# Performance work log

Hardware: AMD Instinct MI355X
Metric: run time of the kernel (lower is better)

Reference implementation:

```python
import jax, jax.numpy as jnp
import numpy as np

V, D, H, L, S, W = 32000, 1024, 16, 2, 2048, 256
HD = D // H
SCALE = 1.0 / np.sqrt(HD)
NEG = -1e30
EPS = 1e-5


def setup_inputs() -> dict:
    key = jax.random.key(0)
    ks = jax.random.split(key, 16)
    f = lambda k, shape, s=0.02: (jax.random.normal(k, shape, jnp.float32) * s)
    return {
        'input_ids': jax.random.randint(ks[0], (1, S), 0, V, jnp.int32),
        'emb': f(ks[1], (V, D)),                 # token embedding, tied lm_head
        'pos_emb': f(ks[2], (S, D)),
        'wq': f(ks[3], (L, D, D)), 'bq': jnp.zeros((L, D), jnp.float32),
        'wk': f(ks[4], (L, D, D)), 'bk': jnp.zeros((L, D), jnp.float32),
        'wv': f(ks[5], (L, D, D)), 'bv': jnp.zeros((L, D), jnp.float32),
        'wo': f(ks[6], (L, D, D)), 'bo': jnp.zeros((L, D), jnp.float32),
        'w1': f(ks[7], (L, D, 4 * D)), 'b1': jnp.zeros((L, 4 * D), jnp.float32),
        'w2': f(ks[8], (L, 4 * D, D)), 'b2': jnp.zeros((L, D), jnp.float32),
        'ln1_g': jnp.ones((L, D), jnp.float32), 'ln1_b': jnp.zeros((L, D), jnp.float32),
        'ln2_g': jnp.ones((L, D), jnp.float32), 'ln2_b': jnp.zeros((L, D), jnp.float32),
        'out_g': jnp.ones((D,), jnp.float32), 'out_b': jnp.zeros((D,), jnp.float32),
    }


def _ln(x, g, b):
    mu = jnp.mean(x, axis=-1, keepdims=True)
    var = jnp.mean(jnp.square(x - mu), axis=-1, keepdims=True)
    return (x - mu) * jax.lax.rsqrt(var + EPS) * g + b


def _forward(input_ids, emb, pos_emb, wq, bq, wk, bk, wv, bv, wo, bo,
             w1, b1, w2, b2, ln1_g, ln1_b, ln2_g, ln2_b, out_g, out_b):
    B, seq = input_ids.shape
    x = emb[input_ids] + pos_emb[None, :seq]  # [B,S,D]
    idx = jnp.arange(seq)
    local_mask = jnp.abs(idx[:, None] - idx[None, :]) <= (W // 2)  # [S,S] band
    for l in range(L):
        h = _ln(x, ln1_g[l], ln1_b[l])
        q = (h @ wq[l] + bq[l]).reshape(B, seq, H, HD)
        k = (h @ wk[l] + bk[l]).reshape(B, seq, H, HD)
        v = (h @ wv[l] + bv[l]).reshape(B, seq, H, HD)
        scores = jnp.einsum('bqhd,bkhd->bhqk', q, k) * SCALE
        scores = jnp.where(local_mask[None, None], scores, NEG)
        attn = jax.nn.softmax(scores, axis=-1)
        o = jnp.einsum('bhqk,bkhd->bqhd', attn, v).reshape(B, seq, D)
        x = x + (o @ wo[l] + bo[l])
        h2 = _ln(x, ln2_g[l], ln2_b[l])
        ffn = jax.nn.gelu(h2 @ w1[l] + b1[l], approximate=False) @ w2[l] + b2[l]
        x = x + ffn
    x = _ln(x, out_g, out_b)
    logits = x @ emb.T  # tied lm_head, no bias
    return logits


def reference(input_ids, emb, pos_emb, wq, bq, wk, bk, wv, bv, wo, bo,
              w1, b1, w2, b2, ln1_g, ln1_b, ln2_g, ln2_b, out_g, out_b):
    return _forward(input_ids, emb, pos_emb, wq, bq, wk, bk, wv, bv, wo, bo,
                    w1, b1, w2, b2, ln1_g, ln1_b, ln2_g, ln2_b, out_g, out_b)
```

## Files before the change

kernel.cpp:

```cpp
#include <hip/hip_runtime.h>
#include <hip/hip_bf16.h>
#include <math.h>

#define SEQ    2048
#define DMODEL 1024
#define NHEAD  16
#define HDIM   64
#define NLAYER 2
#define VOCAB  32000
#define HALFW  128

typedef float  f32x4  __attribute__((ext_vector_type(4)));
typedef short  s16x8  __attribute__((ext_vector_type(8)));

__device__ __forceinline__ unsigned bf16_rne(float x) {
    unsigned b = __builtin_bit_cast(unsigned, x);
    return (b + 0x7FFFu + ((b >> 16) & 1u)) >> 16;
}
__device__ __forceinline__ unsigned pack2(float lo, float hi) {
    return bf16_rne(lo) | (bf16_rne(hi) << 16);
}
__device__ __forceinline__ void gl_lds16(const void* g, void* l) {
    __builtin_amdgcn_global_load_lds(
        (const __attribute__((address_space(1))) unsigned*)g,
        (__attribute__((address_space(3))) unsigned*)l, 16, 0, 0);
}

__global__ __launch_bounds__(256) void embed_kernel(
    const int* __restrict__ ids, const float* __restrict__ emb,
    const float* __restrict__ pos, float* __restrict__ X)
{
    const int s = blockIdx.x;
    const int t = threadIdx.x;
    const int id = ids[s];
    f32x4 e = *(const f32x4*)(emb + (size_t)id * DMODEL + t * 4);
    f32x4 p = *(const f32x4*)(pos + (size_t)s  * DMODEL + t * 4);
    *(f32x4*)(X + (size_t)s * DMODEL + t * 4) = e + p;
}

__global__ __launch_bounds__(256) void convert_bf16_kernel(
    const float* __restrict__ X, unsigned short* __restrict__ Y)
{
    const size_t i = (size_t)blockIdx.x * 256 + threadIdx.x;
    f32x4 a = *(const f32x4*)(X + i * 8);
    f32x4 b = *(const f32x4*)(X + i * 8 + 4);
    uint4 u = make_uint4(pack2(a.x, a.y), pack2(a.z, a.w),
                         pack2(b.x, b.y), pack2(b.z, b.w));
    *(uint4*)(Y + i * 8) = u;
}

__global__ __launch_bounds__(256) void transpose_bf16_kernel(
    const float* __restrict__ W, unsigned short* __restrict__ Wt, int K, int N)
{
    __shared__ unsigned short tile[64][65];
    const int k0 = blockIdx.x * 64;
    const int n0 = blockIdx.y * 64;
    const int t = threadIdx.x;
    const int tr = t >> 6;
    const int tc = t & 63;
    #pragma unroll
    for (int i = 0; i < 16; ++i) {
        int r = i * 4 + tr;
        tile[r][tc] = (unsigned short)bf16_rne(W[(size_t)(k0 + r) * N + n0 + tc]);
    }
    __syncthreads();
    #pragma unroll
    for (int i = 0; i < 16; ++i) {
        int r = i * 4 + tr;
        Wt[(size_t)(n0 + r) * K + k0 + tc] = tile[tc][r];
    }
}

__global__ __launch_bounds__(256) void pack3_kernel(
    const float* __restrict__ a, const float* __restrict__ b,
    const float* __restrict__ c, float* __restrict__ out)
{
    const int i = blockIdx.x * 256 + threadIdx.x;
    float v = (i < 1024) ? a[i] : (i < 2048 ? b[i - 1024] : c[i - 2048]);
    out[i] = v;
}

__global__ __launch_bounds__(256) void ln_bf16_kernel(
    const float* __restrict__ X, const float* __restrict__ G,
    const float* __restrict__ Bb, unsigned short* __restrict__ Y)
{
    const int row = blockIdx.x;
    const int t = threadIdx.x;
    const float* xp = X + (size_t)row * DMODEL;
    f32x4 v = *(const f32x4*)(xp + t * 4);
    float s1 = v.x + v.y + v.z + v.w;
    float s2 = v.x * v.x + v.y * v.y + v.z * v.z + v.w * v.w;
    #pragma unroll
    for (int off = 32; off; off >>= 1) {
        s1 += __shfl_down(s1, off);
        s2 += __shfl_down(s2, off);
    }
    __shared__ float red[8];
    const int wave = t >> 6, lane = t & 63;
    if (lane == 0) { red[wave] = s1; red[wave + 4] = s2; }
    __syncthreads();
    s1 = red[0] + red[1] + red[2] + red[3];
    s2 = red[4] + red[5] + red[6] + red[7];
    const float mu  = s1 * (1.0f / DMODEL);
    const float var = s2 * (1.0f / DMODEL) - mu * mu;
    const float rs  = rsqrtf(var + 1e-5f);
    f32x4 g = *(const f32x4*)(G + t * 4);
    f32x4 b = *(const f32x4*)(Bb + t * 4);
    float y0 = (v.x - mu) * rs * g.x + b.x;
    float y1 = (v.y - mu) * rs * g.y + b.y;
    float y2 = (v.z - mu) * rs * g.z + b.z;
    float y3 = (v.w - mu) * rs * g.w + b.w;
    *(uint2*)(Y + (size_t)row * DMODEL + t * 4) = make_uint2(pack2(y0, y1), pack2(y2, y3));
}

template<int BM, int GELU, int OUT_BF16, int SWZ>
__global__ __launch_bounds__(256) void gemm_bf16(
    const unsigned short* __restrict__ A,
    const unsigned short* __restrict__ Bt,
    const float* __restrict__ bias, const float* __restrict__ resid,
    float* __restrict__ C, unsigned short* __restrict__ Cb,
    int M, int N, int K)
{
    constexpr int MW = BM / 64;
    constexpr int NW = 4 / MW;
    constexpr int WN = 128 / NW;
    constexpr int MI = 4;
    constexpr int NI = WN / 16;

    __shared__ unsigned short As[BM * 32];
    __shared__ unsigned short Bs[128 * 32];

    const int t = threadIdx.x;
    const int wave = t >> 6, lane = t & 63;

    int bx = blockIdx.x, by = blockIdx.y;
    if (SWZ) {
        const int gx = gridDim.x;
        const int nwg = gx * gridDim.y;
        const int flat = by * gx + bx;
        const int chunk = nwg >> 3;
        const int nf = (flat & 7) * chunk + (flat >> 3);
        bx = nf % gx;  by = nf / gx;
    }
    const int m0 = bx * BM;
    const int n0 = by * 128;

    const int wm = (wave % MW) * 64;
    const int wn = (wave / MW) * WN;
    const int lrow = lane & 15, quad = lane >> 4;

    const int ldsub = lane >> 2;
    const int kofs  = (((lane & 3) ^ ((lane >> 3) & 3)) * 8);
    const int rsw   = (lrow >> 1) & 3;

    f32x4 acc[MI][NI] = {};

    const unsigned short* Ap = A + (size_t)m0 * K + kofs;
    const unsigned short* Bp = Bt + (size_t)n0 * K + kofs;

    for (int k0 = 0; k0 < K; k0 += 32) {
        __syncthreads();
        #pragma unroll
        for (int i = 0; i < MW; ++i) {
            const int r = i * 4 + wave;
            gl_lds16(Ap + (size_t)(r * 16 + ldsub) * K + k0, (char*)As + r * 1024);
        }
        #pragma unroll
        for (int i = 0; i < 2; ++i) {
            const int r = i * 4 + wave;
            gl_lds16(Bp + (size_t)(r * 16 + ldsub) * K + k0, (char*)Bs + r * 1024);
        }
        __syncthreads();

        s16x8 af[MI], bfr[NI];
        #pragma unroll
        for (int i = 0; i < MI; ++i)
            af[i] = *(const s16x8*)(As + (wm + i * 16 + lrow) * 32 + ((quad ^ rsw) * 8));
        #pragma unroll
        for (int j = 0; j < NI; ++j)
            bfr[j] = *(const s16x8*)(Bs + (wn + j * 16 + lrow) * 32 + ((quad ^ rsw) * 8));
        #pragma unroll
        for (int i = 0; i < MI; ++i)
            #pragma unroll
            for (int j = 0; j < NI; ++j)
                acc[i][j] = __builtin_amdgcn_mfma_f32_16x16x32_bf16(af[i], bfr[j], acc[i][j], 0, 0, 0);
    }

    #pragma unroll
    for (int j = 0; j < NI; ++j) {
        const int col = n0 + wn + j * 16 + lrow;
        const float bv = bias ? bias[col] : 0.0f;
        #pragma unroll
        for (int i = 0; i < MI; ++i) {
            #pragma unroll
            for (int r = 0; r < 4; ++r) {
                const int row = m0 + wm + i * 16 + quad * 4 + r;
                float vv = acc[i][j][r] + bv;
                if (GELU) vv = 0.5f * vv * (1.0f + erff(vv * 0.70710678118f));
                const size_t off = (size_t)row * N + col;
                if (OUT_BF16) {
                    Cb[off] = (unsigned short)bf16_rne(vv);
                } else {
                    if (resid) vv += resid[off];
                    C[off] = vv;
                }
            }
        }
    }
}

__global__ __launch_bounds__(256) void attn_mfma_kernel(
    const unsigned short* __restrict__ QKV, unsigned short* __restrict__ O)
{
    constexpr int LDK = 72;
    constexpr int LDP = 40;
    __shared__ unsigned short Ks[32 * LDK];
    __shared__ unsigned short Vs[32 * LDK];
    __shared__ unsigned short Pl[4][16 * LDP];

    const int t    = threadIdx.x;
    const int wave = t >> 6;
    const int lane = t & 63;
    const int quad = lane >> 4;
    const int c    = lane & 15;
    const int h    = blockIdx.y;
    const int q0   = blockIdx.x * 64;
    const int qw   = q0 + wave * 16;

    const int srow = t >> 3;
    const int scol = (t & 7) * 8;

    const unsigned short* qrow = QKV + (size_t)(qw + c) * 3072 + h * HDIM;
    const s16x8 qf0 = *(const s16x8*)(qrow + quad * 8);
    const s16x8 qf1 = *(const s16x8*)(qrow + 32 + quad * 8);

    float m = -1e30f, lsum = 0.0f;
    f32x4 oacc[4] = {};
    unsigned short* pb = &Pl[wave][0];

    for (int kb = 0; kb < 10; ++kb) {
        const int kstart = q0 - HALFW + kb * 32;
        __syncthreads();
        {
            const int kc = min(max(kstart + srow, 0), SEQ - 1);
            const unsigned short* kr = QKV + (size_t)kc * 3072 + DMODEL + h * HDIM + scol;
            const uint4 kvv = *(const uint4*)kr;
            const uint4 vvv = *(const uint4*)(kr + DMODEL);
            *(uint4*)(Ks + srow * LDK + scol) = kvv;
            *(uint4*)(Vs + srow * LDK + scol) = vvv;
        }
        __syncthreads();

        if (kstart > qw + 15 + HALFW || kstart + 31 < qw - HALFW ||
            kstart + 31 < 0 || kstart >= SEQ)
            continue;

        f32x4 st0 = {0.f, 0.f, 0.f, 0.f}, st1 = {0.f, 0.f, 0.f, 0.f};
        {
            const s16x8 ka00 = *(const s16x8*)(Ks + c * LDK + quad * 8);
            const s16x8 ka01 = *(const s16x8*)(Ks + c * LDK + 32 + quad * 8);
            const s16x8 ka10 = *(const s16x8*)(Ks + (16 + c) * LDK + quad * 8);
            const s16x8 ka11 = *(const s16x8*)(Ks + (16 + c) * LDK + 32 + quad * 8);
            st0 = __builtin_amdgcn_mfma_f32_16x16x32_bf16(ka00, qf0, st0, 0, 0, 0);
            st0 = __builtin_amdgcn_mfma_f32_16x16x32_bf16(ka01, qf1, st0, 0, 0, 0);
            st1 = __builtin_amdgcn_mfma_f32_16x16x32_bf16(ka10, qf0, st1, 0, 0, 0);
            st1 = __builtin_amdgcn_mfma_f32_16x16x32_bf16(ka11, qf1, st1, 0, 0, 0);
        }

        float sv[8];
        #pragma unroll
        for (int j = 0; j < 8; ++j) {
            const int half = j >> 2, r = j & 3;
            const int key = kstart + half * 16 + quad * 4 + r;
            const int d = key - (qw + c);
            const bool valid = (key >= 0) && (key < SEQ) && (d <= HALFW) && (d >= -HALFW);
            const float s = (half ? st1[r] : st0[r]) * 0.125f;
            sv[j] = valid ? s : -1e30f;
        }
        float tmax = sv[0];
        #pragma unroll
        for (int j = 1; j < 8; ++j) tmax = fmaxf(tmax, sv[j]);
        tmax = fmaxf(tmax, __shfl_xor(tmax, 16));
        tmax = fmaxf(tmax, __shfl_xor(tmax, 32));
        const float mnew = fmaxf(m, tmax);
        const float alpha = __expf(m - mnew);
        m = mnew;

        float p[8], psum = 0.0f;
        #pragma unroll
        for (int j = 0; j < 8; ++j) {
            p[j] = (sv[j] > -1e29f) ? __expf(sv[j] - mnew) : 0.0f;
            psum += p[j];
        }
        psum += __shfl_xor(psum, 16);
        psum += __shfl_xor(psum, 32);
        lsum = lsum * alpha + psum;

        #pragma unroll
        for (int j = 0; j < 8; ++j) {
            const int half = j >> 2, r = j & 3;
            pb[c * LDP + half * 16 + quad * 4 + r] = (unsigned short)bf16_rne(p[j]);
        }

        #pragma unroll
        for (int r = 0; r < 4; ++r) {
            const float ar = __shfl(alpha, quad * 4 + r);
            oacc[0][r] *= ar; oacc[1][r] *= ar; oacc[2][r] *= ar; oacc[3][r] *= ar;
        }

        asm volatile("" ::: "memory");
        const s16x8 pa = *(const s16x8*)(pb + c * LDP + quad * 8);

        #pragma unroll
        for (int dt = 0; dt < 4; ++dt) {
            s16x8 vb;
            #pragma unroll
            for (int i = 0; i < 8; ++i)
                vb[i] = (short)Vs[(quad * 8 + i) * LDK + dt * 16 + c];
            oacc[dt] = __builtin_amdgcn_mfma_f32_16x16x32_bf16(pa, vb, oacc[dt], 0, 0, 0);
        }
    }

    #pragma unroll
    for (int r = 0; r < 4; ++r) {
        const float li = 1.0f / __shfl(lsum, quad * 4 + r);
        unsigned short* op = O + (size_t)(qw + quad * 4 + r) * DMODEL + h * HDIM + c;
        op[0]  = (unsigned short)bf16_rne(oacc[0][r] * li);
        op[16] = (unsigned short)bf16_rne(oacc[1][r] * li);
        op[32] = (unsigned short)bf16_rne(oacc[2][r] * li);
        op[48] = (unsigned short)bf16_rne(oacc[3][r] * li);
    }
}

extern "C" void kernel_launch(void* const* d_in, const int* in_sizes, int n_in,
                              void* d_out, int out_size, void* d_ws, size_t ws_size,
                              hipStream_t stream)
{
    const int*   ids  = (const int*)d_in[0];
    const float* emb  = (const float*)d_in[1];
    const float* pos  = (const float*)d_in[2];
    const float* wq   = (const float*)d_in[3];
    const float* bq   = (const float*)d_in[4];
    const float* wk   = (const float*)d_in[5];
    const float* bk   = (const float*)d_in[6];
    const float* wv   = (const float*)d_in[7];
    const float* bv   = (const float*)d_in[8];
    const float* wo   = (const float*)d_in[9];
    const float* bo   = (const float*)d_in[10];
    const float* w1   = (const float*)d_in[11];
    const float* b1   = (const float*)d_in[12];
    const float* w2   = (const float*)d_in[13];
    const float* b2   = (const float*)d_in[14];
    const float* ln1g = (const float*)d_in[15];
    const float* ln1b = (const float*)d_in[16];
    const float* ln2g = (const float*)d_in[17];
    const float* ln2b = (const float*)d_in[18];
    const float* outg = (const float*)d_in[19];
    const float* outb = (const float*)d_in[20];

    const size_t SD = (size_t)SEQ * DMODEL;
    char* ws = (char*)d_ws;
    float*          x     = (float*)ws;           ws += SD * 4;
    unsigned short* qkvb  = (unsigned short*)ws;  ws += (size_t)SEQ * 3 * DMODEL * 2;
    unsigned short* hb    = (unsigned short*)ws;  ws += SD * 2;
    unsigned short* ob    = (unsigned short*)ws;  ws += SD * 2;
    unsigned short* mid   = (unsigned short*)ws;  ws += (size_t)SEQ * 4 * DMODEL * 2;
    unsigned short* embT  = (unsigned short*)ws;  ws += (size_t)VOCAB * DMODEL * 2;
    unsigned short* wT    = (unsigned short*)ws;  ws += (size_t)4 * DMODEL * DMODEL * 2;
    float*          bias3 = (float*)ws;           ws += 3 * DMODEL * 4;

    const size_t DD  = (size_t)DMODEL * DMODEL;
    const size_t DD4 = (size_t)DMODEL * 4 * DMODEL;

    convert_bf16_kernel<<<(VOCAB * DMODEL) / (256 * 8), 256, 0, stream>>>(emb, embT);

    embed_kernel<<<SEQ, 256, 0, stream>>>(ids, emb, pos, x);

    for (int l = 0; l < NLAYER; ++l) {
        ln_bf16_kernel<<<SEQ, 256, 0, stream>>>(x, ln1g + l * DMODEL, ln1b + l * DMODEL, hb);

        transpose_bf16_kernel<<<dim3(16, 16), 256, 0, stream>>>(wq + l * DD, wT,          DMODEL, DMODEL);
        transpose_bf16_kernel<<<dim3(16, 16), 256, 0, stream>>>(wk + l * DD, wT + DD,     DMODEL, DMODEL);
        transpose_bf16_kernel<<<dim3(16, 16), 256, 0, stream>>>(wv + l * DD, wT + 2 * DD, DMODEL, DMODEL);
        pack3_kernel<<<12, 256, 0, stream>>>(bq + l * DMODEL, bk + l * DMODEL, bv + l * DMODEL, bias3);

        gemm_bf16<128, 0, 1, 1><<<dim3(16, 24), 256, 0, stream>>>(
            hb, wT, bias3, nullptr, nullptr, qkvb, SEQ, 3 * DMODEL, DMODEL);

        attn_mfma_kernel<<<dim3(SEQ / 64, NHEAD), 256, 0, stream>>>(qkvb, ob);

        transpose_bf16_kernel<<<dim3(16, 16), 256, 0, stream>>>(wo + l * DD, wT, DMODEL, DMODEL);
        gemm_bf16<64, 0, 0, 0><<<dim3(32, 8), 256, 0, stream>>>(
            ob, wT, bo + l * DMODEL, x, x, nullptr, SEQ, DMODEL, DMODEL);

        ln_bf16_kernel<<<SEQ, 256, 0, stream>>>(x, ln2g + l * DMODEL, ln2b + l * DMODEL, hb);

        transpose_bf16_kernel<<<dim3(16, 64), 256, 0, stream>>>(w1 + l * DD4, wT, DMODEL, 4 * DMODEL);
        gemm_bf16<128, 1, 1, 1><<<dim3(16, 32), 256, 0, stream>>>(
            hb, wT, b1 + l * 4 * DMODEL, nullptr, nullptr, mid, SEQ, 4 * DMODEL, DMODEL);

        transpose_bf16_kernel<<<dim3(64, 16), 256, 0, stream>>>(w2 + l * DD4, wT, 4 * DMODEL, DMODEL);
        gemm_bf16<64, 0, 0, 0><<<dim3(32, 8), 256, 0, stream>>>(
            mid, wT, b2 + l * DMODEL, x, x, nullptr, SEQ, DMODEL, 4 * DMODEL);
    }

    ln_bf16_kernel<<<SEQ, 256, 0, stream>>>(x, outg, outb, hb);

    gemm_bf16<128, 0, 0, 1><<<dim3(16, VOCAB / 128), 256, 0, stream>>>(
        hb, embT, nullptr, nullptr, (float*)d_out, nullptr, SEQ, VOCAB, DMODEL);
}
```

Measured before the change: 1.128 ms.

## Add 256x256 double-buffered MFMA GEMM for the tied lm_head projection

Replaces the 128-tile GEMM used for the vocab logits with a new 512-thread kernel using 256x256 output tiles. It double-buffers global-to-LDS loads with an XOR swizzle, splits the MFMA work into four barrier-separated phases with raised wave priority, and remaps workgroups for cache locality. The larger tile raises arithmetic intensity for the largest GEMM in the model. In exchange it uses 128KB of LDS, limiting occupancy to one block per CU, and adds many barriers per K-step.

```diff
diff --git a/kernel.cpp b/kernel.cpp
--- a/kernel.cpp
+++ b/kernel.cpp
@@ -204,6 +204,114 @@
                     if (resid) vv += resid[off];
                     C[off] = vv;
                 }
+            }
+        }
+    }
+}
+
+#define PHASE256(mib, nib)                                                     \
+  {                                                                            \
+    s16x8 af[4][2], bfv[2][2];                                                 \
+    _Pragma("unroll") for (int mi = 0; mi < 4; ++mi)                           \
+      _Pragma("unroll") for (int kk = 0; kk < 2; ++kk)                         \
+        af[mi][kk] = *(const s16x8*)(Asb +                                     \
+            (wr * 128 + ((mib)*4 + mi) * 16 + lrow) * 64 +                     \
+            (((kk * 4 + quad) ^ r7) * 8));                                     \
+    _Pragma("unroll") for (int ni = 0; ni < 2; ++ni)                           \
+      _Pragma("unroll") for (int kk = 0; kk < 2; ++kk)                         \
+        bfv[ni][kk] = *(const s16x8*)(Bsb +                                    \
+            (wc * 64 + ((nib)*2 + ni) * 16 + lrow) * 64 +                      \
+            (((kk * 4 + quad) ^ r7) * 8));                                     \
+    __builtin_amdgcn_s_barrier();                                              \
+    asm volatile("s_waitcnt lgkmcnt(0)" ::: "memory");                         \
+    __builtin_amdgcn_sched_barrier(0);                                         \
+    __builtin_amdgcn_s_setprio(1);                                             \
+    _Pragma("unroll") for (int mi = 0; mi < 4; ++mi)                           \
+      _Pragma("unroll") for (int ni = 0; ni < 2; ++ni)                         \
+        _Pragma("unroll") for (int kk = 0; kk < 2; ++kk)                       \
+          acc[(mib)*4 + mi][(nib)*2 + ni] =                                    \
+              __builtin_amdgcn_mfma_f32_16x16x32_bf16(                         \
+                  af[mi][kk], bfv[ni][kk], acc[(mib)*4 + mi][(nib)*2 + ni],    \
+                  0, 0, 0);                                                    \
+    __builtin_amdgcn_s_setprio(0);                                             \
+    __builtin_amdgcn_sched_barrier(0);                                         \
+    __builtin_amdgcn_s_barrier();                                              \
+  }
+
+__global__ __launch_bounds__(512) void gemm256_bf16(
+    const unsigned short* __restrict__ A,
+    const unsigned short* __restrict__ Bt,
+    float* __restrict__ C, int M, int N, int K)
+{
+    __shared__ unsigned short As[2][256 * 64];
+    __shared__ unsigned short Bs[2][256 * 64];
+
+    const int t = threadIdx.x;
+    const int wave = t >> 6, lane = t & 63;
+    const int wr = wave >> 2, wc = wave & 3;
+    const int lrow = lane & 15, quad = lane >> 4;
+    const int r7 = lrow & 7;
+
+    int bx = blockIdx.x, by = blockIdx.y;
+    {
+        const int gx = gridDim.x;
+        const int nwg = gx * gridDim.y;
+        const int flat = by * gx + bx;
+        const int chunk = nwg >> 3;
+        const int nf = (flat & 7) * chunk + (flat >> 3);
+        bx = nf % gx;  by = nf / gx;
+    }
+    const int m0 = bx * 256;
+    const int n0 = by * 256;
+
+    const int grow = lane >> 3;
+    const int gchk = (lane & 7) ^ grow;
+    const unsigned short* Ag = A + (size_t)(m0 + grow) * K + gchk * 8;
+    const unsigned short* Bg = Bt + (size_t)(n0 + grow) * K + gchk * 8;
+
+    f32x4 acc[8][4] = {};
+
+    const int NT = K >> 6;
+
+    #pragma unroll
+    for (int i = 0; i < 4; ++i) {
+        const int ga = i * 8 + wave;
+        gl_lds16(Ag + (size_t)(8 * ga) * K, (char*)&As[0][0] + ga * 1024);
+        gl_lds16(Bg + (size_t)(8 * ga) * K, (char*)&Bs[0][0] + ga * 1024);
+    }
+
+    int buf = 0;
+    for (int kt = 0; kt < NT; ++kt) {
+        asm volatile("s_waitcnt vmcnt(0)" ::: "memory");
+        __builtin_amdgcn_s_barrier();
+        __builtin_amdgcn_sched_barrier(0);
+        if (kt + 1 < NT) {
+            const size_t kof = (size_t)(kt + 1) * 64;
+            #pragma unroll
+            for (int i = 0; i < 4; ++i) {
+                const int ga = i * 8 + wave;
+                gl_lds16(Ag + (size_t)(8 * ga) * K + kof, (char*)&As[buf ^ 1][0] + ga * 1024);
+                gl_lds16(Bg + (size_t)(8 * ga) * K + kof, (char*)&Bs[buf ^ 1][0] + ga * 1024);
+            }
+        }
+        const unsigned short* Asb = &As[buf][0];
+        const unsigned short* Bsb = &Bs[buf][0];
+        PHASE256(0, 0)
+        PHASE256(0, 1)
+        PHASE256(1, 0)
+        PHASE256(1, 1)
+        buf ^= 1;
+    }
+
+    #pragma unroll
+    for (int mi = 0; mi < 8; ++mi) {
+        #pragma unroll
+        for (int ni = 0; ni < 4; ++ni) {
+            const int col = n0 + wc * 64 + ni * 16 + lrow;
+            #pragma unroll
+            for (int r = 0; r < 4; ++r) {
+                const int row = m0 + wr * 128 + mi * 16 + quad * 4 + r;
+                C[(size_t)row * N + col] = acc[mi][ni][r];
             }
         }
     }
@@ -406,6 +514,6 @@
 
     ln_bf16_kernel<<<SEQ, 256, 0, stream>>>(x, outg, outb, hb);
 
-    gemm_bf16<128, 0, 0, 1><<<dim3(16, VOCAB / 128), 256, 0, stream>>>(
-        hb, embT, nullptr, nullptr, (float*)d_out, nullptr, SEQ, VOCAB, DMODEL);
-}
+    gemm256_bf16<<<dim3(SEQ / 256, VOCAB / 256), 512, 0, stream>>>(
+        hb, embT, (float*)d_out, SEQ, VOCAB, DMODEL);
+}
```

Result: faster. 1.084 ms (-3.9%).
